# Performance work log

Measured on AMD Instinct MI355X. Metric: run time of the kernel, lower is better.

Reference implementation:

```python
import jax, jax.numpy as jnp
import numpy as np

C = 64
DQK = C // 8  # query/key channels


def setup_inputs() -> dict:
    key = jax.random.key(0)
    ks = jax.random.split(key, 8)
    B, H, W = 4, 64, 64
    x = jax.random.normal(ks[0], (B, C, H, W), dtype=jnp.float32)
    # 1x1 conv weights stored as (out_ch, in_ch); biases as (out_ch,)
    wq = jax.random.normal(ks[1], (DQK, C), dtype=jnp.float32) * 0.05
    bq = jnp.zeros((DQK,), dtype=jnp.float32)
    wk = jax.random.normal(ks[2], (DQK, C), dtype=jnp.float32) * 0.05
    bk = jnp.zeros((DQK,), dtype=jnp.float32)
    wv = jax.random.normal(ks[3], (C, C), dtype=jnp.float32) * 0.05
    bv = jnp.zeros((C,), dtype=jnp.float32)
    gamma = jnp.zeros((1,), dtype=jnp.float32)
    return {"x": x, "wq": wq, "bq": bq, "wk": wk, "bk": bk,
            "wv": wv, "bv": bv, "gamma": gamma}


def reference(x, wq, bq, wk, bk, wv, bv, gamma):
    B, Cc, H, W = x.shape
    N = H * W
    xf = x.reshape(B, Cc, N)  # (B, C, N)
    # 1x1 convs == channel-wise matmuls
    q = jnp.einsum('oc,bcn->bon', wq, xf) + bq[None, :, None]  # (B, dqk, N)
    k = jnp.einsum('oc,bcn->bon', wk, xf) + bk[None, :, None]  # (B, dqk, N)
    v = jnp.einsum('oc,bcn->bon', wv, xf) + bv[None, :, None]  # (B, C, N)
    # qk = q^T k -> (B, N, N), softmax over last dim
    qk = jnp.einsum('bdn,bdm->bnm', q, k)
    attn = jax.nn.softmax(qk, axis=-1)
    # out = v @ attn^T : out[b,c,i] = sum_j v[b,c,j] * attn[b,i,j]
    out = jnp.einsum('bcj,bij->bci', v, attn)
    out = out.reshape(B, Cc, H, W)
    return gamma * out + x
```

## Files before the change

### kernel.cpp

```cpp
#include <hip/hip_runtime.h>
#include <cmath>

namespace {

constexpr int B = 4;
constexpr int C = 64;
constexpr int N = 4096;
constexpr float LOG2E = 1.4426950408889634f;

typedef __bf16 bf16x8 __attribute__((ext_vector_type(8)));
typedef float f32x16 __attribute__((ext_vector_type(16)));
typedef float f32x2 __attribute__((ext_vector_type(2)));
typedef unsigned short u16;

union B8 {
  int4 i;
  bf16x8 h;
  unsigned int w[4];
};

__device__ inline u16 f2bf(float f) {
  unsigned int u = __float_as_uint(f);
  u += 0x7FFFu + ((u >> 16) & 1u);
  return (u16)(u >> 16);
}

__device__ inline unsigned int cvt_pk_bf16(float lo, float hi) {
  unsigned int r;
  asm("v_cvt_pk_bf16_f32 %0, %1, %2" : "=v"(r) : "v"(lo), "v"(hi));
  return r;
}

__device__ inline f32x2 pk_add(f32x2 a, f32x2 b) {
  f32x2 r;
  asm("v_pk_add_f32 %0, %1, %2" : "=v"(r) : "v"(a), "v"(b));
  return r;
}

__device__ inline float exp2_fast(float x) {
#if __has_builtin(__builtin_amdgcn_exp2f)
  return __builtin_amdgcn_exp2f(x);
#else
  return exp2f(x);
#endif
}

__device__ __host__ inline int sigma4(int j) {
  return (j & 3) | ((j & 4) << 1) | ((j & 8) >> 1);
}

__global__ __launch_bounds__(1024) void qkv_kernel(
    const float* __restrict__ x,
    const float* __restrict__ wq, const float* __restrict__ bq,
    const float* __restrict__ wk, const float* __restrict__ bk,
    const float* __restrict__ wv, const float* __restrict__ bv,
    u16* __restrict__ qt, u16* __restrict__ kt, u16* __restrict__ vo) {
  const int bid = blockIdx.x;
  const int xcd = bid & 7;
  const int b = xcd >> 1;
  const int nt = (xcd & 1) * 32 + (bid >> 3);
  const int t = threadIdx.x;
  const int nn = t & 63;
  const int wid = __builtin_amdgcn_readfirstlane(t >> 6);
  const int n0 = nt * 64;
  const int n = n0 + nn;

  __shared__ float x_s[64][66];

  const float* xb = x + (size_t)b * C * N + n0;
  #pragma unroll
  for (int i = 0; i < 4; ++i) {
    const int idx = t + i * 1024;
    const int c = idx >> 6, j = idx & 63;
    x_s[j][c] = xb[(size_t)c * N + j];
  }
  __syncthreads();

  const int c0 = wid * 4;
  float a0 = bv[c0], a1 = bv[c0 + 1], a2 = bv[c0 + 2], a3 = bv[c0 + 3];
  const float* wqk = (wid < 8) ? (wq + wid * C) : (wk + (wid - 8) * C);
  float aqk = (wid < 8) ? bq[wid] : bk[wid - 8];

  #pragma unroll 8
  for (int c = 0; c < C; c += 2) {
    const f32x2 xv = *reinterpret_cast<const f32x2*>(&x_s[nn][c]);
    a0 = fmaf(wv[(c0 + 0) * C + c], xv.x, fmaf(wv[(c0 + 0) * C + c + 1], xv.y, a0));
    a1 = fmaf(wv[(c0 + 1) * C + c], xv.x, fmaf(wv[(c0 + 1) * C + c + 1], xv.y, a1));
    a2 = fmaf(wv[(c0 + 2) * C + c], xv.x, fmaf(wv[(c0 + 2) * C + c + 1], xv.y, a2));
    a3 = fmaf(wv[(c0 + 3) * C + c], xv.x, fmaf(wv[(c0 + 3) * C + c + 1], xv.y, a3));
    aqk = fmaf(wqk[c], xv.x, fmaf(wqk[c + 1], xv.y, aqk));
  }

  if (wid < 8)
    qt[((size_t)b * N + n) * 8 + wid] = f2bf(aqk * LOG2E);
  else
    kt[((size_t)b * N + n) * 8 + (wid - 8)] = f2bf(aqk);

  const int sj = sigma4(n & 15);
  const size_t tb = ((size_t)b * (N / 16) + (n >> 4)) * (C * 16) + sj;
  vo[tb + (size_t)(c0 + 0) * 16] = f2bf(a0);
  vo[tb + (size_t)(c0 + 1) * 16] = f2bf(a1);
  vo[tb + (size_t)(c0 + 2) * 16] = f2bf(a2);
  vo[tb + (size_t)(c0 + 3) * 16] = f2bf(a3);
}

__global__ __launch_bounds__(512, 2) void attn_kernel(
    const u16* __restrict__ qt, const u16* __restrict__ kt,
    const u16* __restrict__ vv, const float* __restrict__ x,
    const float* __restrict__ gamma, float* __restrict__ out) {
  const int bid = blockIdx.x;
  const int xcd = bid & 7;
  const int b = xcd >> 1;
  const int i0 = ((xcd & 1) * 64 + (bid >> 3)) * 32;
  const int t = threadIdx.x;
  const int lane = t & 63;
  const int w = __builtin_amdgcn_readfirstlane(t >> 6);
  const int il = lane & 31;
  const int hi = lane >> 5;

  __shared__ float l_lds[8][32];
  __shared__ u16 o_lds[8][32][66];

  B8 qf;
  if (hi == 0)
    qf.i = *reinterpret_cast<const int4*>(qt + ((size_t)b * N + i0 + il) * 8);
  else
    qf.i = make_int4(0, 0, 0, 0);

  const u16* kbase = kt + (size_t)b * N * 8 + ((size_t)w * 512 + il) * 8;
  const u16* vbase = vv + (size_t)b * (N / 16) * (C * 16) +
                     (size_t)w * 32 * (C * 16) + il * 16 + hi * 8;

  f32x16 accA, accB, zero16;
  #pragma unroll
  for (int r = 0; r < 16; ++r) { accA[r] = 0.f; accB[r] = 0.f; zero16[r] = 0.f; }
  f32x2 lrun2 = {0.f, 0.f};

  B8 kf[2], va0[2], va1[2];

  kf[0].i = *reinterpret_cast<const int4*>(kbase);
  va0[0].i = *reinterpret_cast<const int4*>(vbase);
  va1[0].i = *reinterpret_cast<const int4*>(vbase + 1024);
  kf[1].i = *reinterpret_cast<const int4*>(kbase + 256);

  #pragma unroll
  for (int jt = 0; jt < 16; ++jt) {
    const int cur = jt & 1, nxt = (jt + 1) & 1;
    const u16* vp = vbase + jt * 2048;
    f32x16 S =
        __builtin_amdgcn_mfma_f32_32x32x16_bf16(kf[cur].h, qf.h, zero16, 0, 0, 0);
    B8 vb0, vb1;
    vb0.i = *reinterpret_cast<const int4*>(vp + 512);
    vb1.i = *reinterpret_cast<const int4*>(vp + 1536);
    if (jt + 1 < 16) {
      va0[nxt].i = *reinterpret_cast<const int4*>(vp + 2048);
      va1[nxt].i = *reinterpret_cast<const int4*>(vp + 3072);
    }
    if (jt + 2 < 16)
      kf[cur].i = *reinterpret_cast<const int4*>(kbase + (jt + 2) * 256);
    float p[16];
    #pragma unroll
    for (int r = 0; r < 16; ++r) p[r] = exp2_fast(S[r]);
    B8 pf0, pf1;
    pf0.w[0] = cvt_pk_bf16(p[0], p[1]);
    pf0.w[1] = cvt_pk_bf16(p[2], p[3]);
    pf0.w[2] = cvt_pk_bf16(p[4], p[5]);
    pf0.w[3] = cvt_pk_bf16(p[6], p[7]);
    pf1.w[0] = cvt_pk_bf16(p[8], p[9]);
    pf1.w[1] = cvt_pk_bf16(p[10], p[11]);
    pf1.w[2] = cvt_pk_bf16(p[12], p[13]);
    pf1.w[3] = cvt_pk_bf16(p[14], p[15]);
    accA = __builtin_amdgcn_mfma_f32_32x32x16_bf16(va0[cur].h, pf0.h, accA, 0, 0, 0);
    accA = __builtin_amdgcn_mfma_f32_32x32x16_bf16(va1[cur].h, pf1.h, accA, 0, 0, 0);
    accB = __builtin_amdgcn_mfma_f32_32x32x16_bf16(vb0.h, pf0.h, accB, 0, 0, 0);
    accB = __builtin_amdgcn_mfma_f32_32x32x16_bf16(vb1.h, pf1.h, accB, 0, 0, 0);
    const f32x2* u = reinterpret_cast<const f32x2*>(p);
    f32x2 s0 = pk_add(u[0], u[1]);
    f32x2 s1 = pk_add(u[2], u[3]);
    f32x2 s2 = pk_add(u[4], u[5]);
    f32x2 s3 = pk_add(u[6], u[7]);
    s0 = pk_add(s0, s1);
    s2 = pk_add(s2, s3);
    lrun2 = pk_add(lrun2, pk_add(s0, s2));
  }

  const float lr = lrun2.x + lrun2.y;
  const float lw = lr + __shfl_xor(lr, 32);
  if (hi == 0) l_lds[w][il] = lw;
  #pragma unroll
  for (int r = 0; r < 16; r += 2) {
    const int c = (r & 3) + 8 * (r >> 2) + 4 * hi;
    *reinterpret_cast<unsigned int*>(&o_lds[w][il][c]) =
        cvt_pk_bf16(accA[r], accA[r + 1]);
    *reinterpret_cast<unsigned int*>(&o_lds[w][il][c + 32]) =
        cvt_pk_bf16(accB[r], accB[r + 1]);
  }
  __syncthreads();

  const int i = t & 31;
  float Li = 0.f;
  #pragma unroll
  for (int ww = 0; ww < 8; ++ww) Li += l_lds[ww][i];
  const float ginv = gamma[0] / Li;

  #pragma unroll
  for (int q4 = 0; q4 < 4; ++q4) {
    const int flat = t + q4 * 512;
    const int c = flat >> 5;
    float s = 0.f;
    #pragma unroll
    for (int ww = 0; ww < 8; ++ww)
      s += __uint_as_float((unsigned int)o_lds[ww][i][c] << 16);
    const size_t off = ((size_t)b * C + c) * N + i0 + i;
    out[off] = fmaf(ginv, s, x[off]);
  }
}

}

extern "C" void kernel_launch(void* const* d_in, const int* in_sizes, int n_in,
                              void* d_out, int out_size, void* d_ws, size_t ws_size,
                              hipStream_t stream) {
  const float* x     = (const float*)d_in[0];
  const float* wq    = (const float*)d_in[1];
  const float* bq    = (const float*)d_in[2];
  const float* wk    = (const float*)d_in[3];
  const float* bk    = (const float*)d_in[4];
  const float* wv    = (const float*)d_in[5];
  const float* bv    = (const float*)d_in[6];
  const float* gamma = (const float*)d_in[7];
  float* out = (float*)d_out;

  u16* qt = (u16*)d_ws;
  u16* kt = qt + (size_t)B * N * 8;
  u16* vo = kt + (size_t)B * N * 8;

  qkv_kernel<<<B * (N / 64), 1024, 0, stream>>>(x, wq, bq, wk, bk, wv, bv, qt, kt, vo);
  attn_kernel<<<B * (N / 32), 512, 0, stream>>>(qt, kt, vo, x, gamma, out);
}
```

Baseline: 26.72 us.

## Process two query tiles per attention block to reuse K/V loads

Each attention block now handles 64 query rows, as two 32-row sub-tiles, instead of 32. Every loaded K and V fragment feeds both sub-tiles, which halves global K/V traffic per query, and the grid shrinks to 256 blocks. The epilogue runs twice with LDS reuse. The cost is more accumulator registers, which may lower occupancy under launch_bounds(512,2), and fewer blocks to spread across CUs.

```diff
diff --git a/kernel.cpp b/kernel.cpp
--- a/kernel.cpp
+++ b/kernel.cpp
@@ -111,7 +111,7 @@
   const int bid = blockIdx.x;
   const int xcd = bid & 7;
   const int b = xcd >> 1;
-  const int i0 = ((xcd & 1) * 64 + (bid >> 3)) * 32;
+  const int i0 = ((xcd & 1) * 32 + (bid >> 3)) * 64;
   const int t = threadIdx.x;
   const int lane = t & 63;
   const int w = __builtin_amdgcn_readfirstlane(t >> 6);
@@ -121,20 +121,26 @@
   __shared__ float l_lds[8][32];
   __shared__ u16 o_lds[8][32][66];
 
-  B8 qf;
-  if (hi == 0)
-    qf.i = *reinterpret_cast<const int4*>(qt + ((size_t)b * N + i0 + il) * 8);
-  else
-    qf.i = make_int4(0, 0, 0, 0);
+  B8 qf0, qf1;
+  if (hi == 0) {
+    qf0.i = *reinterpret_cast<const int4*>(qt + ((size_t)b * N + i0 + il) * 8);
+    qf1.i = *reinterpret_cast<const int4*>(qt + ((size_t)b * N + i0 + 32 + il) * 8);
+  } else {
+    qf0.i = make_int4(0, 0, 0, 0);
+    qf1.i = make_int4(0, 0, 0, 0);
+  }
 
   const u16* kbase = kt + (size_t)b * N * 8 + ((size_t)w * 512 + il) * 8;
   const u16* vbase = vv + (size_t)b * (N / 16) * (C * 16) +
                      (size_t)w * 32 * (C * 16) + il * 16 + hi * 8;
 
-  f32x16 accA, accB, zero16;
+  f32x16 accA0, accB0, accA1, accB1, zero16;
   #pragma unroll
-  for (int r = 0; r < 16; ++r) { accA[r] = 0.f; accB[r] = 0.f; zero16[r] = 0.f; }
-  f32x2 lrun2 = {0.f, 0.f};
+  for (int r = 0; r < 16; ++r) {
+    accA0[r] = 0.f; accB0[r] = 0.f; accA1[r] = 0.f; accB1[r] = 0.f;
+    zero16[r] = 0.f;
+  }
+  f32x2 lrun0 = {0.f, 0.f}, lrun1 = {0.f, 0.f};
 
   B8 kf[2], va0[2], va1[2];
 
@@ -143,12 +149,36 @@
   va1[0].i = *reinterpret_cast<const int4*>(vbase + 1024);
   kf[1].i = *reinterpret_cast<const int4*>(kbase + 256);
 
+  auto SMPACK = [&](const f32x16& S, f32x2& lrun, B8& pf0, B8& pf1) {
+    float p[16];
+    #pragma unroll
+    for (int r = 0; r < 16; ++r) p[r] = exp2_fast(S[r]);
+    pf0.w[0] = cvt_pk_bf16(p[0], p[1]);
+    pf0.w[1] = cvt_pk_bf16(p[2], p[3]);
+    pf0.w[2] = cvt_pk_bf16(p[4], p[5]);
+    pf0.w[3] = cvt_pk_bf16(p[6], p[7]);
+    pf1.w[0] = cvt_pk_bf16(p[8], p[9]);
+    pf1.w[1] = cvt_pk_bf16(p[10], p[11]);
+    pf1.w[2] = cvt_pk_bf16(p[12], p[13]);
+    pf1.w[3] = cvt_pk_bf16(p[14], p[15]);
+    const f32x2* u = reinterpret_cast<const f32x2*>(p);
+    f32x2 s0 = pk_add(u[0], u[1]);
+    f32x2 s1 = pk_add(u[2], u[3]);
+    f32x2 s2 = pk_add(u[4], u[5]);
+    f32x2 s3 = pk_add(u[6], u[7]);
+    s0 = pk_add(s0, s1);
+    s2 = pk_add(s2, s3);
+    lrun = pk_add(lrun, pk_add(s0, s2));
+  };
+
   #pragma unroll
   for (int jt = 0; jt < 16; ++jt) {
     const int cur = jt & 1, nxt = (jt + 1) & 1;
     const u16* vp = vbase + jt * 2048;
-    f32x16 S =
-        __builtin_amdgcn_mfma_f32_32x32x16_bf16(kf[cur].h, qf.h, zero16, 0, 0, 0);
+    f32x16 S0 =
+        __builtin_amdgcn_mfma_f32_32x32x16_bf16(kf[cur].h, qf0.h, zero16, 0, 0, 0);
+    f32x16 S1 =
+        __builtin_amdgcn_mfma_f32_32x32x16_bf16(kf[cur].h, qf1.h, zero16, 0, 0, 0);
     B8 vb0, vb1;
     vb0.i = *reinterpret_cast<const int4*>(vp + 512);
     vb1.i = *reinterpret_cast<const int4*>(vp + 1536);
@@ -158,61 +188,59 @@
     }
     if (jt + 2 < 16)
       kf[cur].i = *reinterpret_cast<const int4*>(kbase + (jt + 2) * 256);
-    float p[16];
-    #pragma unroll
-    for (int r = 0; r < 16; ++r) p[r] = exp2_fast(S[r]);
-    B8 pf0, pf1;
-    pf0.w[0] = cvt_pk_bf16(p[0], p[1]);
-    pf0.w[1] = cvt_pk_bf16(p[2], p[3]);
-    pf0.w[2] = cvt_pk_bf16(p[4], p[5]);
-    pf0.w[3] = cvt_pk_bf16(p[6], p[7]);
-    pf1.w[0] = cvt_pk_bf16(p[8], p[9]);
-    pf1.w[1] = cvt_pk_bf16(p[10], p[11]);
-    pf1.w[2] = cvt_pk_bf16(p[12], p[13]);
-    pf1.w[3] = cvt_pk_bf16(p[14], p[15]);
-    accA = __builtin_amdgcn_mfma_f32_32x32x16_bf16(va0[cur].h, pf0.h, accA, 0, 0, 0);
-    accA = __builtin_amdgcn_mfma_f32_32x32x16_bf16(va1[cur].h, pf1.h, accA, 0, 0, 0);
-    accB = __builtin_amdgcn_mfma_f32_32x32x16_bf16(vb0.h, pf0.h, accB, 0, 0, 0);
-    accB = __builtin_amdgcn_mfma_f32_32x32x16_bf16(vb1.h, pf1.h, accB, 0, 0, 0);
-    const f32x2* u = reinterpret_cast<const f32x2*>(p);
-    f32x2 s0 = pk_add(u[0], u[1]);
-    f32x2 s1 = pk_add(u[2], u[3]);
-    f32x2 s2 = pk_add(u[4], u[5]);
-    f32x2 s3 = pk_add(u[6], u[7]);
-    s0 = pk_add(s0, s1);
-    s2 = pk_add(s2, s3);
-    lrun2 = pk_add(lrun2, pk_add(s0, s2));
-  }
-
-  const float lr = lrun2.x + lrun2.y;
-  const float lw = lr + __shfl_xor(lr, 32);
-  if (hi == 0) l_lds[w][il] = lw;
-  #pragma unroll
-  for (int r = 0; r < 16; r += 2) {
-    const int c = (r & 3) + 8 * (r >> 2) + 4 * hi;
-    *reinterpret_cast<unsigned int*>(&o_lds[w][il][c]) =
-        cvt_pk_bf16(accA[r], accA[r + 1]);
-    *reinterpret_cast<unsigned int*>(&o_lds[w][il][c + 32]) =
-        cvt_pk_bf16(accB[r], accB[r + 1]);
-  }
-  __syncthreads();
-
-  const int i = t & 31;
-  float Li = 0.f;
-  #pragma unroll
-  for (int ww = 0; ww < 8; ++ww) Li += l_lds[ww][i];
-  const float ginv = gamma[0] / Li;
-
-  #pragma unroll
-  for (int q4 = 0; q4 < 4; ++q4) {
-    const int flat = t + q4 * 512;
-    const int c = flat >> 5;
-    float s = 0.f;
-    #pragma unroll
-    for (int ww = 0; ww < 8; ++ww)
-      s += __uint_as_float((unsigned int)o_lds[ww][i][c] << 16);
-    const size_t off = ((size_t)b * C + c) * N + i0 + i;
-    out[off] = fmaf(ginv, s, x[off]);
+    B8 pA0, pA1, pB0, pB1;
+    SMPACK(S0, lrun0, pA0, pA1);
+    SMPACK(S1, lrun1, pB0, pB1);
+    accA0 = __builtin_amdgcn_mfma_f32_32x32x16_bf16(va0[cur].h, pA0.h, accA0, 0, 0, 0);
+    accA0 = __builtin_amdgcn_mfma_f32_32x32x16_bf16(va1[cur].h, pA1.h, accA0, 0, 0, 0);
+    accA1 = __builtin_amdgcn_mfma_f32_32x32x16_bf16(va0[cur].h, pB0.h, accA1, 0, 0, 0);
+    accA1 = __builtin_amdgcn_mfma_f32_32x32x16_bf16(va1[cur].h, pB1.h, accA1, 0, 0, 0);
+    accB0 = __builtin_amdgcn_mfma_f32_32x32x16_bf16(vb0.h, pA0.h, accB0, 0, 0, 0);
+    accB0 = __builtin_amdgcn_mfma_f32_32x32x16_bf16(vb1.h, pA1.h, accB0, 0, 0, 0);
+    accB1 = __builtin_amdgcn_mfma_f32_32x32x16_bf16(vb0.h, pB0.h, accB1, 0, 0, 0);
+    accB1 = __builtin_amdgcn_mfma_f32_32x32x16_bf16(vb1.h, pB1.h, accB1, 0, 0, 0);
+  }
+
+  const float lr0 = lrun0.x + lrun0.y;
+  const float lr1 = lrun1.x + lrun1.y;
+  const float lw0 = lr0 + __shfl_xor(lr0, 32);
+  const float lw1 = lr1 + __shfl_xor(lr1, 32);
+  const float g = gamma[0];
+
+  #pragma unroll 2
+  for (int ph = 0; ph < 2; ++ph) {
+    const f32x16& aA = ph ? accA1 : accA0;
+    const f32x16& aB = ph ? accB1 : accB0;
+    const float lw = ph ? lw1 : lw0;
+    __syncthreads();
+    if (hi == 0) l_lds[w][il] = lw;
+    #pragma unroll
+    for (int r = 0; r < 16; r += 2) {
+      const int c = (r & 3) + 8 * (r >> 2) + 4 * hi;
+      *reinterpret_cast<unsigned int*>(&o_lds[w][il][c]) =
+          cvt_pk_bf16(aA[r], aA[r + 1]);
+      *reinterpret_cast<unsigned int*>(&o_lds[w][il][c + 32]) =
+          cvt_pk_bf16(aB[r], aB[r + 1]);
+    }
+    __syncthreads();
+
+    const int i = t & 31;
+    float Li = 0.f;
+    #pragma unroll
+    for (int ww = 0; ww < 8; ++ww) Li += l_lds[ww][i];
+    const float ginv = g / Li;
+
+    #pragma unroll
+    for (int q4 = 0; q4 < 4; ++q4) {
+      const int flat = t + q4 * 512;
+      const int c = flat >> 5;
+      float s = 0.f;
+      #pragma unroll
+      for (int ww = 0; ww < 8; ++ww)
+        s += __uint_as_float((unsigned int)o_lds[ww][i][c] << 16);
+      const size_t off = ((size_t)b * C + c) * N + i0 + ph * 32 + i;
+      out[off] = fmaf(ginv, s, x[off]);
+    }
   }
 }
 
@@ -236,5 +264,5 @@
   u16* vo = kt + (size_t)B * N * 8;
 
   qkv_kernel<<<B * (N / 64), 1024, 0, stream>>>(x, wq, bq, wk, bk, wv, bv, qt, kt, vo);
-  attn_kernel<<<B * (N / 32), 512, 0, stream>>>(qt, kt, vo, x, gamma, out);
-}
+  attn_kernel<<<B * (N / 64), 512, 0, stream>>>(qt, kt, vo, x, gamma, out);
+}
```

Result: faster. 25.37 us (-5.1%).
